# Kernel optimization log

Measured on AMD Instinct MI355X. Metric: run time of the kernel, lower is better.

Reference implementation:

```python
import jax, jax.numpy as jnp
import numpy as np

B, S, E = 8, 4096, 768
NEG = jnp.float32(-1e30)


def setup_inputs() -> dict:
    key = jax.random.key(0)
    ks = jax.random.split(key, 9)
    full_ebd = jax.random.normal(ks[0], (B, S, E), dtype=jnp.float32)
    # first_idx in [64, S//2): end of question span (question tokens are 1..first_idx-1)
    first = jax.random.randint(ks[1], (B,), 64, S // 2)
    # second_idx in (first, S): end of context span (unused by the math but part of API)
    second = jax.random.randint(ks[2], (B,), S // 2 + 1, S)
    SEQ_idxes = jnp.stack([first, second], axis=1).astype(jnp.int64)
    w = 0.02
    Wq_w = jax.random.normal(ks[3], (E, E), dtype=jnp.float32) * w
    Wq_b = jax.random.normal(ks[4], (E,), dtype=jnp.float32) * w
    Wk_w = jax.random.normal(ks[5], (E, E), dtype=jnp.float32) * w
    Wk_b = jax.random.normal(ks[6], (E,), dtype=jnp.float32) * w
    Wv_w = jax.random.normal(ks[7], (E, E), dtype=jnp.float32) * w
    Wv_b = jax.random.normal(ks[8], (E,), dtype=jnp.float32) * w
    return {"full_ebd": full_ebd, "SEQ_idxes": SEQ_idxes,
            "Wq_w": Wq_w, "Wq_b": Wq_b, "Wk_w": Wk_w, "Wk_b": Wk_b,
            "Wv_w": Wv_w, "Wv_b": Wv_b}


def reference(full_ebd, SEQ_idxes, Wq_w, Wq_b, Wk_w, Wk_b, Wv_w, Wv_b):
    # Vectorized form of the ragged per-sample loop: queries attend to the
    # question tokens 1..first_idx-1 only; masking keys reproduces the slice.
    seq = full_ebd.shape[1]
    inv_sqrt_dk = jnp.float32(1.0 / np.sqrt(full_ebd.shape[-1]))
    Q = full_ebd @ Wq_w.T + Wq_b              # [B,S,E]
    K = full_ebd @ Wk_w.T + Wk_b              # [B,S,E]
    V = full_ebd @ Wv_w.T + Wv_b              # [B,S,E]
    first = SEQ_idxes[:, 0]                   # [B]
    j = jnp.arange(seq)
    key_mask = (j[None, :] >= 1) & (j[None, :] < first[:, None])  # [B,S]
    scores = jnp.einsum('bqe,bke->bqk', Q, K) * inv_sqrt_dk       # [B,S,S]
    scores = jnp.where(key_mask[:, None, :], scores, NEG)
    attn = jax.nn.softmax(scores, axis=-1)
    attn = attn * key_mask[:, None, :].astype(attn.dtype)  # exact zeros outside span
    H = jnp.einsum('bqk,bke->bqe', attn, V)   # [B,S,E]
    return H
```

## Files before the change

kernel.cpp:

```cpp
#include <hip/hip_runtime.h>
#include <hip/hip_bf16.h>
#include <cmath>

typedef __bf16 bf16x8 __attribute__((ext_vector_type(8)));
typedef __bf16 bf16x4 __attribute__((ext_vector_type(4)));
typedef float f32x4 __attribute__((ext_vector_type(4)));

#define GLOBAL_AS __attribute__((address_space(1)))
#define LDS_AS __attribute__((address_space(3)))

__device__ __forceinline__ void async_copy16(const void* g, void* l) {
    __builtin_amdgcn_global_load_lds((const GLOBAL_AS void*)g, (LDS_AS void*)l, 16, 0, 0);
}

#define BB 8
#define SS 4096
#define EE 768
#define SKK 2048

__device__ inline int get_first(const int* __restrict__ seq, int b) {
    int stride = (seq[1] == 0) ? 4 : 2;
    return seq[b * stride];
}

__global__ __launch_bounds__(256) void cast_f32_bf16(const float* __restrict__ in,
                                                     __bf16* __restrict__ out, int n4) {
    int i = blockIdx.x * 256 + threadIdx.x;
    if (i >= n4) return;
    float4 v = ((const float4*)in)[i];
    bf16x4 o;
    o[0] = (__bf16)v.x; o[1] = (__bf16)v.y; o[2] = (__bf16)v.z; o[3] = (__bf16)v.w;
    ((bf16x4*)out)[i] = o;
}

__global__ __launch_bounds__(256) void cast3_f32_bf16(
    const float* __restrict__ a, const float* __restrict__ b, const float* __restrict__ c,
    __bf16* __restrict__ oa, __bf16* __restrict__ ob, __bf16* __restrict__ oc, int n4) {
    int i = blockIdx.x * 256 + threadIdx.x;
    if (i >= n4) return;
    const float* in = (blockIdx.y == 0) ? a : (blockIdx.y == 1) ? b : c;
    __bf16* out = (blockIdx.y == 0) ? oa : (blockIdx.y == 1) ? ob : oc;
    float4 v = ((const float4*)in)[i];
    bf16x4 o;
    o[0] = (__bf16)v.x; o[1] = (__bf16)v.y; o[2] = (__bf16)v.z; o[3] = (__bf16)v.w;
    ((bf16x4*)out)[i] = o;
}

__global__ __launch_bounds__(256) void zero_f32(float* __restrict__ p, int n4) {
    int i = blockIdx.x * 256 + threadIdx.x;
    if (i < n4) ((f32x4*)p)[i] = f32x4{0.f, 0.f, 0.f, 0.f};
}

__device__ __forceinline__ void gemm_core(
    const __bf16* __restrict__ A0, int lda,
    const __bf16* __restrict__ B0, int ldb, int K,
    char* As, char* Bs, f32x4 (&acc)[4][4]) {
    int tid = threadIdx.x;
    int lane = tid & 63, wid = tid >> 6;
    int waveM = (wid & 1) << 6, waveN = (wid >> 1) << 6;
    int quad = lane >> 4, l16 = lane & 15;
    int r0 = tid >> 3;
    int c8 = (tid & 7) ^ (r0 & 7);
    const __bf16* Ag = A0 + (long)r0 * lda + c8 * 8;
    const __bf16* Bg = B0 + (long)r0 * ldb + c8 * 8;
#pragma unroll
    for (int i = 0; i < 4; ++i)
#pragma unroll
        for (int j = 0; j < 4; ++j) acc[i][j] = f32x4{0.f, 0.f, 0.f, 0.f};
    int xorv = (l16 & 7) << 4;

    for (int k0 = 0; k0 < K; k0 += 64) {
        __syncthreads();
#pragma unroll
        for (int r = 0; r < 4; ++r) {
            async_copy16(Ag + (long)(r * 32) * lda + k0, As + (tid + r * 256) * 16);
            async_copy16(Bg + (long)(r * 32) * ldb + k0, Bs + (tid + r * 256) * 16);
        }
        __syncthreads();
#pragma unroll
        for (int s = 0; s < 2; ++s) {
            bf16x8 af[4], bfr[4];
#pragma unroll
            for (int i = 0; i < 4; ++i) {
                int chunk = (((s << 2) + quad) << 4) ^ xorv;
                af[i]  = *(const bf16x8*)(As + (waveM + i * 16 + l16) * 128 + chunk);
                bfr[i] = *(const bf16x8*)(Bs + (waveN + i * 16 + l16) * 128 + chunk);
            }
#pragma unroll
            for (int i = 0; i < 4; ++i)
#pragma unroll
                for (int j = 0; j < 4; ++j)
                    acc[i][j] = __builtin_amdgcn_mfma_f32_16x16x32_bf16(af[i], bfr[j], acc[i][j], 0, 0, 0);
        }
    }
}


__global__ __launch_bounds__(256) void proj_qkv(
    const __bf16* __restrict__ ebd,
    const __bf16* __restrict__ wq, const __bf16* __restrict__ wk, const __bf16* __restrict__ wv,
    const float* __restrict__ bq, const float* __restrict__ bk, const float* __restrict__ bv,
    __bf16* __restrict__ Qb, __bf16* __restrict__ Kb, __bf16* __restrict__ VT,
    const int* __restrict__ seq, int* __restrict__ ctr) {
    __shared__ char As[16384];
    __shared__ char Bs[16384];
    __shared__ int s_id;
    int tid = threadIdx.x;
    int lane = tid & 63, wid = tid >> 6;
    int waveM = (wid & 1) << 6, waveN = (wid >> 1) << 6;
    int quad = lane >> 4, l16 = lane & 15;

    for (;;) {
        __syncthreads();
        if (tid == 0) s_id = atomicAdd(ctr, 1);
        __syncthreads();
        int id = s_id;
        if (id >= 3072) return;

        int which, m0, n0, z;
        if (id < 1536) {
            which = 0; m0 = (id & 31) << 7; n0 = ((id >> 5) % 6) << 7; z = id / 192;
        } else {
            int rel = id - 1536;
            which = 1 + rel / 768; rel %= 768;
            m0 = (rel & 15) << 7; n0 = ((rel >> 4) % 6) << 7; z = rel / 96;
            if (m0 >= get_first(seq, z)) continue;
        }
        const __bf16* W = (which == 0) ? wq : (which == 1) ? wk : wv;
        const float* bias = (which == 0) ? bq : (which == 1) ? bk : bv;

        f32x4 acc[4][4];
        gemm_core(ebd + (long)z * SS * EE + (long)m0 * EE, EE, W + (long)n0 * EE, EE,
                  EE, As, Bs, acc);

        if (which == 2) {
            __bf16* C = VT + (long)z * EE * SKK;
#pragma unroll
            for (int i = 0; i < 4; ++i) {
                int rowb = m0 + waveM + i * 16 + quad * 4;
#pragma unroll
                for (int j = 0; j < 4; ++j) {
                    int col = n0 + waveN + j * 16 + l16;
                    float bv_ = bias[col];
                    bf16x4 o;
#pragma unroll
                    for (int r = 0; r < 4; ++r) o[r] = (__bf16)(acc[i][j][r] + bv_);
                    *(bf16x4*)&C[(long)col * SKK + rowb] = o;
                }
            }
        } else {
            __bf16* C = (which == 0) ? Qb + (long)z * SS * EE : Kb + (long)z * SKK * EE;
#pragma unroll
            for (int i = 0; i < 4; ++i) {
                int rowb = m0 + waveM + i * 16 + quad * 4;
#pragma unroll
                for (int j = 0; j < 4; ++j) {
                    int col = n0 + waveN + j * 16 + l16;
                    float bv_ = bias[col];
#pragma unroll
                    for (int r = 0; r < 4; ++r)
                        C[(long)(rowb + r) * EE + col] = (__bf16)(acc[i][j][r] + bv_);
                }
            }
        }
    }
}

__global__ __launch_bounds__(256) void scores_k(
    const __bf16* __restrict__ Qb, const __bf16* __restrict__ Kb,
    __bf16* __restrict__ Pb, const int* __restrict__ seq,
    float* __restrict__ rowsum, int* __restrict__ ctr) {
    __shared__ char As[16384];
    __shared__ char Bs[16384];
    __shared__ int s_id;
    int tid = threadIdx.x;
    int lane = tid & 63, wid = tid >> 6;
    int waveM = (wid & 1) << 6, waveN = (wid >> 1) << 6;
    int quad = lane >> 4, l16 = lane & 15;
    const float cs = 1.44269504088896f / 27.712812921102035f;

    for (;;) {
        __syncthreads();
        if (tid == 0) s_id = atomicAdd(ctr, 1);
        __syncthreads();
        int id = s_id;
        if (id >= 4096) return;
        int m0 = (id & 31) << 7, n0 = ((id >> 5) & 15) << 7, z = id >> 9;
        int first = get_first(seq, z);
        if (n0 >= first) continue;

        f32x4 acc[4][4];
        gemm_core(Qb + (long)z * SS * EE + (long)m0 * EE, EE,
                  Kb + (long)z * SKK * EE + (long)n0 * EE, EE, EE, As, Bs, acc);

        __bf16* C = Pb + (long)z * SS * SKK;
        float* rs = rowsum + (long)z * SS;
#pragma unroll
        for (int i = 0; i < 4; ++i) {
            int rowb = m0 + waveM + i * 16 + quad * 4;
            float sum[4] = {0.f, 0.f, 0.f, 0.f};
#pragma unroll
            for (int j = 0; j < 4; ++j) {
                int col = n0 + waveN + j * 16 + l16;
                bool valid = (col >= 1) && (col < first);
#pragma unroll
                for (int r = 0; r < 4; ++r) {
                    float e = valid ? exp2f(acc[i][j][r] * cs) : 0.0f;
                    __bf16 pb = (__bf16)e;
                    C[(long)(rowb + r) * SKK + col] = pb;
                    sum[r] += (float)pb;
                }
            }
#pragma unroll
            for (int r = 0; r < 4; ++r) {
                float v = sum[r];
                v += __shfl_xor(v, 8); v += __shfl_xor(v, 4);
                v += __shfl_xor(v, 2); v += __shfl_xor(v, 1);
                if (l16 == 0) atomicAdd(&rs[rowb + r], v);
            }
        }
    }
}

__global__ __launch_bounds__(256) void pv_k(
    const __bf16* __restrict__ Pb, const __bf16* __restrict__ VT,
    float* __restrict__ out, const float* __restrict__ rowsum,
    const int* __restrict__ seq, int* __restrict__ ctr) {
    __shared__ char As[16384];
    __shared__ char Bs[16384];
    __shared__ int s_id;
    int tid = threadIdx.x;
    int lane = tid & 63, wid = tid >> 6;
    int waveM = (wid & 1) << 6, waveN = (wid >> 1) << 6;
    int quad = lane >> 4, l16 = lane & 15;

    for (;;) {
        __syncthreads();
        if (tid == 0) s_id = atomicAdd(ctr, 1);
        __syncthreads();
        int id = s_id;
        if (id >= 1536) return;
        int m0 = (id & 31) << 7;
        int t = id >> 5;
        int n0 = (t % 6) << 7, z = t / 6;
        int K = (get_first(seq, z) + 63) & ~63;

        f32x4 acc[4][4];
        gemm_core(Pb + (long)z * SS * SKK + (long)m0 * SKK, SKK,
                  VT + (long)z * EE * SKK + (long)n0 * SKK, SKK, K, As, Bs, acc);

        float* C = out + (long)z * SS * EE;
        const float* rs = rowsum + (long)z * SS;
#pragma unroll
        for (int i = 0; i < 4; ++i) {
            int rowb = m0 + waveM + i * 16 + quad * 4;
            float inv[4];
#pragma unroll
            for (int r = 0; r < 4; ++r) inv[r] = 1.0f / rs[rowb + r];
#pragma unroll
            for (int j = 0; j < 4; ++j) {
                int col = n0 + waveN + j * 16 + l16;
#pragma unroll
                for (int r = 0; r < 4; ++r)
                    C[(long)(rowb + r) * EE + col] = acc[i][j][r] * inv[r];
            }
        }
    }
}

extern "C" void kernel_launch(void* const* d_in, const int* in_sizes, int n_in,
                              void* d_out, int out_size, void* d_ws, size_t ws_size,
                              hipStream_t stream) {
    const int B = BB, S = SS, E = EE, SK = SKK;
    const float* ebd  = (const float*)d_in[0];
    const int*   seq  = (const int*)d_in[1];
    const float* Wq_w = (const float*)d_in[2];
    const float* Wq_b = (const float*)d_in[3];
    const float* Wk_w = (const float*)d_in[4];
    const float* Wk_b = (const float*)d_in[5];
    const float* Wv_w = (const float*)d_in[6];
    const float* Wv_b = (const float*)d_in[7];
    float* out = (float*)d_out;

    char* p = (char*)d_ws;
    __bf16* ebd_bf = (__bf16*)p; p += (size_t)B * S * E * 2;
    __bf16* wq = (__bf16*)p;     p += (size_t)E * E * 2;
    __bf16* wk = (__bf16*)p;     p += (size_t)E * E * 2;
    __bf16* wv = (__bf16*)p;     p += (size_t)E * E * 2;
    __bf16* Qb = (__bf16*)p;     p += (size_t)B * S * E * 2;
    __bf16* Kb = (__bf16*)p;     p += (size_t)B * SK * E * 2;
    __bf16* VT = (__bf16*)p;     p += (size_t)B * E * SK * 2;
    __bf16* Pb = (__bf16*)p;     p += (size_t)B * S * SK * 2;
    float* rowsum = (float*)p;   p += (size_t)B * S * 4;
    int* ctrs = (int*)p;         p += 256;

    zero_f32<<<(B * S / 4 + 64 + 255) / 256, 256, 0, stream>>>(rowsum, B * S / 4 + 64);
    cast_f32_bf16<<<(B * S * E / 4 + 255) / 256, 256, 0, stream>>>(ebd, ebd_bf, B * S * E / 4);
    cast3_f32_bf16<<<dim3((E * E / 4 + 255) / 256, 3), 256, 0, stream>>>(
        Wq_w, Wk_w, Wv_w, wq, wk, wv, E * E / 4);

    const int NB = 1280;
    proj_qkv<<<NB, 256, 0, stream>>>(ebd_bf, wq, wk, wv, Wq_b, Wk_b, Wv_b,
                                     Qb, Kb, VT, seq, ctrs + 0);
    scores_k<<<NB, 256, 0, stream>>>(Qb, Kb, Pb, seq, rowsum, ctrs + 1);
    pv_k<<<NB, 256, 0, stream>>>(Pb, VT, out, rowsum, seq, ctrs + 2);
}
```

Baseline: 472.6 us.

## Reorder tile scheduling for L2 reuse and raise occupancy to five blocks

Changes the work-item to tile mapping in all three GEMM kernels so consecutive dynamically-scheduled tiles share the same A row-block (N varies fastest) or form small M-by-N supertiles, which should improve L2 reuse of the activation and probability tiles. It also adds a min-blocks-per-CU hint of 5 to launch_bounds. Finally, the work-id broadcast now goes through the A shared buffer instead of a separate shared int, saving a few bytes of LDS so five blocks fit. The occupancy hint may force register spilling.

Measured after the change: 621.7 us. 1.32x slower.

```diff
diff --git a/kernel.cpp b/kernel.cpp
--- a/kernel.cpp
+++ b/kernel.cpp
@@ -49,6 +49,13 @@
 __global__ __launch_bounds__(256) void zero_f32(float* __restrict__ p, int n4) {
     int i = blockIdx.x * 256 + threadIdx.x;
     if (i < n4) ((f32x4*)p)[i] = f32x4{0.f, 0.f, 0.f, 0.f};
+}
+
+__device__ __forceinline__ int next_item(int* ctr, char* As) {
+    __syncthreads();
+    if (threadIdx.x == 0) *(int*)As = atomicAdd(ctr, 1);
+    __syncthreads();
+    return *(const int*)As;
 }
 
 __device__ __forceinline__ void gemm_core(
@@ -96,7 +103,7 @@
 }
 
 
-__global__ __launch_bounds__(256) void proj_qkv(
+__global__ __launch_bounds__(256, 5) void proj_qkv(
     const __bf16* __restrict__ ebd,
     const __bf16* __restrict__ wq, const __bf16* __restrict__ wk, const __bf16* __restrict__ wv,
     const float* __restrict__ bq, const float* __restrict__ bk, const float* __restrict__ bv,
@@ -104,26 +111,23 @@
     const int* __restrict__ seq, int* __restrict__ ctr) {
     __shared__ char As[16384];
     __shared__ char Bs[16384];
-    __shared__ int s_id;
     int tid = threadIdx.x;
     int lane = tid & 63, wid = tid >> 6;
     int waveM = (wid & 1) << 6, waveN = (wid >> 1) << 6;
     int quad = lane >> 4, l16 = lane & 15;
 
     for (;;) {
-        __syncthreads();
-        if (tid == 0) s_id = atomicAdd(ctr, 1);
-        __syncthreads();
-        int id = s_id;
+        int id = next_item(ctr, As);
         if (id >= 3072) return;
 
         int which, m0, n0, z;
         if (id < 1536) {
-            which = 0; m0 = (id & 31) << 7; n0 = ((id >> 5) % 6) << 7; z = id / 192;
+            which = 0;
+            n0 = (id % 6) << 7; int t = id / 6; m0 = (t & 31) << 7; z = t >> 5;
         } else {
             int rel = id - 1536;
             which = 1 + rel / 768; rel %= 768;
-            m0 = (rel & 15) << 7; n0 = ((rel >> 4) % 6) << 7; z = rel / 96;
+            n0 = (rel % 6) << 7; int t = rel / 6; m0 = (t & 15) << 7; z = t >> 4;
             if (m0 >= get_first(seq, z)) continue;
         }
         const __bf16* W = (which == 0) ? wq : (which == 1) ? wk : wv;
@@ -166,13 +170,12 @@
     }
 }
 
-__global__ __launch_bounds__(256) void scores_k(
+__global__ __launch_bounds__(256, 5) void scores_k(
     const __bf16* __restrict__ Qb, const __bf16* __restrict__ Kb,
     __bf16* __restrict__ Pb, const int* __restrict__ seq,
     float* __restrict__ rowsum, int* __restrict__ ctr) {
     __shared__ char As[16384];
     __shared__ char Bs[16384];
-    __shared__ int s_id;
     int tid = threadIdx.x;
     int lane = tid & 63, wid = tid >> 6;
     int waveM = (wid & 1) << 6, waveN = (wid >> 1) << 6;
@@ -180,12 +183,10 @@
     const float cs = 1.44269504088896f / 27.712812921102035f;
 
     for (;;) {
-        __syncthreads();
-        if (tid == 0) s_id = atomicAdd(ctr, 1);
-        __syncthreads();
-        int id = s_id;
+        int id = next_item(ctr, As);
         if (id >= 4096) return;
-        int m0 = (id & 31) << 7, n0 = ((id >> 5) & 15) << 7, z = id >> 9;
+        int mloc = id & 3, n0 = ((id >> 2) & 15) << 7, msup = (id >> 6) & 7, z = id >> 9;
+        int m0 = (msup * 4 + mloc) << 7;
         int first = get_first(seq, z);
         if (n0 >= first) continue;
 
@@ -222,27 +223,23 @@
     }
 }
 
-__global__ __launch_bounds__(256) void pv_k(
+__global__ __launch_bounds__(256, 5) void pv_k(
     const __bf16* __restrict__ Pb, const __bf16* __restrict__ VT,
     float* __restrict__ out, const float* __restrict__ rowsum,
     const int* __restrict__ seq, int* __restrict__ ctr) {
     __shared__ char As[16384];
     __shared__ char Bs[16384];
-    __shared__ int s_id;
     int tid = threadIdx.x;
     int lane = tid & 63, wid = tid >> 6;
     int waveM = (wid & 1) << 6, waveN = (wid >> 1) << 6;
     int quad = lane >> 4, l16 = lane & 15;
 
     for (;;) {
-        __syncthreads();
-        if (tid == 0) s_id = atomicAdd(ctr, 1);
-        __syncthreads();
-        int id = s_id;
+        int id = next_item(ctr, As);
         if (id >= 1536) return;
-        int m0 = (id & 31) << 7;
-        int t = id >> 5;
-        int n0 = (t % 6) << 7, z = t / 6;
+        int n0 = (id % 6) << 7;
+        int t = id / 6;
+        int m0 = (t & 31) << 7, z = t >> 5;
         int K = (get_first(seq, z) + 63) & ~63;
 
         f32x4 acc[4][4];
```
